# Performance work log

Hardware: AMD Instinct MI355X
Metric: run time of the kernel (lower is better)

The kernel has to match this reference:

```python
import jax, jax.numpy as jnp
import numpy as np

VOCAB, EMBED, CONV_C, HID, LABELS = 50257, 512, 512, 1024, 128
B, S = 32, 1024

def setup_inputs() -> dict:
    key = jax.random.key(0)
    ks = jax.random.split(key, 8)
    sc = lambda d: 1.0 / np.sqrt(d)
    return {
        "token_ids": jax.random.randint(ks[0], (B, S), 0, VOCAB),
        "emb_table": jax.random.normal(ks[1], (VOCAB, EMBED), jnp.float32) * 0.02,
        "conv_w": jax.random.normal(ks[2], (CONV_C, EMBED), jnp.float32) * sc(EMBED),
        "conv_b": jnp.zeros((CONV_C,), jnp.float32),
        "dec_w1": jax.random.normal(ks[3], (CONV_C, HID), jnp.float32) * sc(CONV_C),
        "dec_b1": jnp.zeros((HID,), jnp.float32),
        "dec_w2": jax.random.normal(ks[4], (HID, LABELS), jnp.float32) * sc(HID),
        "dec_b2": jnp.zeros((LABELS,), jnp.float32),
    }

def reference(token_ids, emb_table, conv_w, conv_b, dec_w1, dec_b1, dec_w2, dec_b2):
    # Embedding lookup: [B, S, E]
    x = emb_table[token_ids]
    # DocNN encoder on a length-1 sequence = kernel-1 conv + relu (+ trivial max-over-time)
    h = jax.nn.relu(jnp.einsum('bse,ce->bsc', x, conv_w) + conv_b)  # [B,S,C]
    # MLP decoder per word
    z = jax.nn.relu(jnp.einsum('bsc,ch->bsh', h, dec_w1) + dec_b1)  # [B,S,H]
    logits = jnp.einsum('bsh,hl->bsl', z, dec_w2) + dec_b2          # [B,S,L]
    # torch.cat over dim 0 of per-word outputs -> flat [B*S, L]
    return logits.reshape(-1, logits.shape[-1])
```

## Files before the change

### kernel.cpp

```cpp
#include <hip/hip_runtime.h>

typedef __bf16 bf16;
typedef __bf16 bf16x4 __attribute__((ext_vector_type(4)));
typedef __bf16 bf16x8 __attribute__((ext_vector_type(8)));
typedef float f32x4 __attribute__((ext_vector_type(4)));

#define NROWS 32768
#define EMBED 512
#define CONV_C 512
#define HID 1024
#define LABELS 128

__device__ inline void async16(const void* g, void* l) {
  __builtin_amdgcn_global_load_lds(
      (const __attribute__((address_space(1))) void*)g,
      (__attribute__((address_space(3))) void*)l, 16, 0, 0);
}

__device__ inline bf16x8 cvt8(const float* p) {
  f32x4 lo = *(const f32x4*)p;
  f32x4 hi = *(const f32x4*)(p + 4);
  bf16x8 r;
  r[0] = (bf16)lo[0]; r[1] = (bf16)lo[1]; r[2] = (bf16)lo[2]; r[3] = (bf16)lo[3];
  r[4] = (bf16)hi[0]; r[5] = (bf16)hi[1]; r[6] = (bf16)hi[2]; r[7] = (bf16)hi[3];
  return r;
}

__global__ void transpose_cvt(const float* __restrict__ in, bf16* __restrict__ out,
                              int K, int N) {
  __shared__ float t[64][65];
  int kb = blockIdx.x * 64, nb = blockIdx.y * 64;
  for (int i = threadIdx.x; i < 4096; i += 256) {
    int r = i >> 6, c = i & 63;
    t[r][c] = in[(size_t)(kb + r) * N + nb + c];
  }
  __syncthreads();
  for (int i = threadIdx.x; i < 4096; i += 256) {
    int r = i >> 6, c = i & 63;
    out[(size_t)(nb + r) * K + kb + c] = (bf16)t[c][r];
  }
}

__global__ __launch_bounds__(256) void gemm1_gather(
    const int* __restrict__ tok, const float* __restrict__ emb,
    const float* __restrict__ convw, const float* __restrict__ bias,
    bf16* __restrict__ out, int M, int N, int K) {
  __shared__ __attribute__((aligned(16))) float lAf[128 * 32];
  __shared__ __attribute__((aligned(16))) float lBf[128 * 32];
  const int tid = threadIdx.x;
  const int wave = tid >> 6, lane = tid & 63;
  const int m0 = blockIdx.x * 128, n0 = blockIdx.y * 128;
  const int wm = (wave & 1) * 64, wn = (wave >> 1) * 64;
  const int lrow = lane & 15, quad = lane >> 4;
  const int slot0 = wave * 64 + lane;
  const int cs4 = (slot0 & 7) * 4;
  const int rbase = slot0 >> 3;

  int trow[4];
#pragma unroll
  for (int c = 0; c < 4; ++c) trow[c] = tok[m0 + rbase + c * 32];

  const f32x4 zero4 = {0.f, 0.f, 0.f, 0.f};
  f32x4 acc[4][4];
#pragma unroll
  for (int i = 0; i < 4; ++i)
#pragma unroll
    for (int j = 0; j < 4; ++j) acc[i][j] = zero4;

  for (int k0 = 0; k0 < K; k0 += 32) {
#pragma unroll
    for (int c = 0; c < 4; ++c) {
      int row = rbase + c * 32;
      async16(emb + (size_t)trow[c] * EMBED + k0 + cs4,
              lAf + (size_t)(wave * 64 + c * 256) * 4);
      async16(convw + (size_t)(n0 + row) * K + k0 + cs4,
              lBf + (size_t)(wave * 64 + c * 256) * 4);
    }
    __syncthreads();

    bf16x8 a[4], b[4];
#pragma unroll
    for (int t = 0; t < 4; ++t) {
      a[t] = cvt8(lAf + (wm + t * 16 + lrow) * 32 + quad * 8);
      b[t] = cvt8(lBf + (wn + t * 16 + lrow) * 32 + quad * 8);
    }
#pragma unroll
    for (int mi = 0; mi < 4; ++mi)
#pragma unroll
      for (int ni = 0; ni < 4; ++ni)
        acc[mi][ni] =
            __builtin_amdgcn_mfma_f32_16x16x32_bf16(a[mi], b[ni], acc[mi][ni], 0, 0, 0);
    __syncthreads();
  }

#pragma unroll
  for (int mi = 0; mi < 4; ++mi) {
#pragma unroll
    for (int ni = 0; ni < 4; ++ni) {
      int col = n0 + wn + ni * 16 + lrow;
      float bv = bias[col];
#pragma unroll
      for (int r = 0; r < 4; ++r) {
        int row = m0 + wm + mi * 16 + quad * 4 + r;
        float v = acc[mi][ni][r] + bv;
        v = v > 0.f ? v : 0.f;
        out[(size_t)row * N + col] = (bf16)v;
      }
    }
  }
}

template <int BK, bool RELU, bool OUTBF>
__global__ __launch_bounds__(256) void gemm_bt(const bf16* __restrict__ A,
                                               const bf16* __restrict__ Bt,
                                               const float* __restrict__ bias,
                                               void* __restrict__ out,
                                               int M, int N, int K) {
  constexpr int GR = BK / 8;
  constexpr int ISS = 128 * GR / 256;
  __shared__ __attribute__((aligned(16))) bf16 lA[128 * BK];
  __shared__ __attribute__((aligned(16))) bf16 lB[128 * BK];
  const int tid = threadIdx.x;
  const int wave = tid >> 6, lane = tid & 63;
  const int m0 = blockIdx.x * 128, n0 = blockIdx.y * 128;
  const int wm = (wave & 1) * 64, wn = (wave >> 1) * 64;
  const int lrow = lane & 15, quad = lane >> 4;
  const int slot0 = wave * 64 + lane;

  const f32x4 zero4 = {0.f, 0.f, 0.f, 0.f};
  f32x4 acc[4][4];
#pragma unroll
  for (int i = 0; i < 4; ++i)
#pragma unroll
    for (int j = 0; j < 4; ++j) acc[i][j] = zero4;

  for (int k0 = 0; k0 < K; k0 += BK) {
#pragma unroll
    for (int c = 0; c < ISS; ++c) {
      int g = slot0 + c * 256;
      int row = g / GR, cs = g % GR;
      async16(A + (size_t)(m0 + row) * K + k0 + cs * 8,
              lA + (size_t)(wave * 64 + c * 256) * 8);
      async16(Bt + (size_t)(n0 + row) * K + k0 + cs * 8,
              lB + (size_t)(wave * 64 + c * 256) * 8);
    }
    __syncthreads();

#pragma unroll
    for (int ks = 0; ks < BK / 32; ++ks) {
      bf16x8 a[4], b[4];
#pragma unroll
      for (int t = 0; t < 4; ++t) {
        a[t] = *(const bf16x8*)(lA + (wm + t * 16 + lrow) * BK + ks * 32 + quad * 8);
        b[t] = *(const bf16x8*)(lB + (wn + t * 16 + lrow) * BK + ks * 32 + quad * 8);
      }
#pragma unroll
      for (int mi = 0; mi < 4; ++mi)
#pragma unroll
        for (int ni = 0; ni < 4; ++ni)
          acc[mi][ni] =
              __builtin_amdgcn_mfma_f32_16x16x32_bf16(a[mi], b[ni], acc[mi][ni], 0, 0, 0);
    }
    __syncthreads();
  }

#pragma unroll
  for (int mi = 0; mi < 4; ++mi) {
#pragma unroll
    for (int ni = 0; ni < 4; ++ni) {
      int col = n0 + wn + ni * 16 + lrow;
      float bv = bias[col];
#pragma unroll
      for (int r = 0; r < 4; ++r) {
        int row = m0 + wm + mi * 16 + quad * 4 + r;
        float v = acc[mi][ni][r] + bv;
        if (RELU) v = v > 0.f ? v : 0.f;
        if (OUTBF)
          ((bf16*)out)[(size_t)row * N + col] = (bf16)v;
        else
          ((float*)out)[(size_t)row * N + col] = v;
      }
    }
  }
}

__global__ __launch_bounds__(256) void gemm_bt64(const bf16* __restrict__ A,
                                                 const bf16* __restrict__ Bt,
                                                 const float* __restrict__ bias,
                                                 float* __restrict__ out,
                                                 int M, int N, int K) {
  __shared__ __attribute__((aligned(16))) bf16 lA[64 * 32];
  __shared__ __attribute__((aligned(16))) bf16 lB[128 * 32];
  const int tid = threadIdx.x;
  const int wave = tid >> 6, lane = tid & 63;
  const int m0 = blockIdx.x * 64, n0 = 0;
  const int wm = (wave & 1) * 32, wn = (wave >> 1) * 64;
  const int lrow = lane & 15, quad = lane >> 4;
  const int slot0 = wave * 64 + lane;

  const f32x4 zero4 = {0.f, 0.f, 0.f, 0.f};
  f32x4 acc[2][4];
#pragma unroll
  for (int i = 0; i < 2; ++i)
#pragma unroll
    for (int j = 0; j < 4; ++j) acc[i][j] = zero4;

  for (int k0 = 0; k0 < K; k0 += 32) {
    {
      int row = slot0 >> 2, cs = slot0 & 3;
      async16(A + (size_t)(m0 + row) * K + k0 + cs * 8,
              lA + (size_t)(wave * 64) * 8);
    }
#pragma unroll
    for (int c = 0; c < 2; ++c) {
      int g = slot0 + c * 256;
      int row = g >> 2, cs = g & 3;
      async16(Bt + (size_t)(n0 + row) * K + k0 + cs * 8,
              lB + (size_t)(wave * 64 + c * 256) * 8);
    }
    __syncthreads();

    bf16x8 a[2], b[4];
#pragma unroll
    for (int t = 0; t < 2; ++t)
      a[t] = *(const bf16x8*)(lA + (wm + t * 16 + lrow) * 32 + quad * 8);
#pragma unroll
    for (int t = 0; t < 4; ++t)
      b[t] = *(const bf16x8*)(lB + (wn + t * 16 + lrow) * 32 + quad * 8);
#pragma unroll
    for (int mi = 0; mi < 2; ++mi)
#pragma unroll
      for (int ni = 0; ni < 4; ++ni)
        acc[mi][ni] =
            __builtin_amdgcn_mfma_f32_16x16x32_bf16(a[mi], b[ni], acc[mi][ni], 0, 0, 0);
    __syncthreads();
  }

#pragma unroll
  for (int mi = 0; mi < 2; ++mi) {
#pragma unroll
    for (int ni = 0; ni < 4; ++ni) {
      int col = n0 + wn + ni * 16 + lrow;
      float bv = bias[col];
#pragma unroll
      for (int r = 0; r < 4; ++r) {
        int row = m0 + wm + mi * 16 + quad * 4 + r;
        out[(size_t)row * N + col] = acc[mi][ni][r] + bv;
      }
    }
  }
}


extern "C" void kernel_launch(void* const* d_in, const int* in_sizes, int n_in,
                              void* d_out, int out_size, void* d_ws, size_t ws_size,
                              hipStream_t stream) {
  const int* tok = (const int*)d_in[0];
  const float* emb = (const float*)d_in[1];
  const float* conv_w = (const float*)d_in[2];
  const float* conv_b = (const float*)d_in[3];
  const float* w1 = (const float*)d_in[4];
  const float* b1 = (const float*)d_in[5];
  const float* w2 = (const float*)d_in[6];
  const float* b2 = (const float*)d_in[7];
  float* out = (float*)d_out;

  char* ws = (char*)d_ws;
  bf16* wt1 = (bf16*)(ws);
  bf16* wt2 = (bf16*)(ws + (1u << 20));
  bf16* h = (bf16*)(ws + (2u << 20));
  bf16* z = (bf16*)(ws + (34u << 20));

  hipLaunchKernelGGL(transpose_cvt, dim3(8, 16), dim3(256), 0, stream,
                     w1, wt1, CONV_C, HID);
  hipLaunchKernelGGL(transpose_cvt, dim3(16, 2), dim3(256), 0, stream,
                     w2, wt2, HID, LABELS);

  hipLaunchKernelGGL(gemm1_gather, dim3(NROWS / 128, CONV_C / 128), dim3(256),
                     0, stream, tok, emb, conv_w, conv_b, h, NROWS, CONV_C, EMBED);
  hipLaunchKernelGGL((gemm_bt<64, true, true>), dim3(NROWS / 128, HID / 128), dim3(256),
                     0, stream, h, wt1, b1, (void*)z, NROWS, HID, CONV_C);
  hipLaunchKernelGGL(gemm_bt64, dim3(NROWS / 64, 1), dim3(256),
                     0, stream, z, wt2, b2, out, NROWS, LABELS, HID);
}
```

Baseline: 290.6 us.

## Pre-convert conv weights to bf16, XOR-swizzle gathered A tile, shrink GEMM2 K-tile

```diff
diff --git a/kernel.cpp b/kernel.cpp
--- a/kernel.cpp
+++ b/kernel.cpp
@@ -17,13 +17,23 @@
       (__attribute__((address_space(3))) void*)l, 16, 0, 0);
 }
 
-__device__ inline bf16x8 cvt8(const float* p) {
-  f32x4 lo = *(const f32x4*)p;
-  f32x4 hi = *(const f32x4*)(p + 4);
+__device__ inline bf16x8 cvt8_sw(const float* row, int o0, int o1) {
+  f32x4 lo = *(const f32x4*)(row + o0);
+  f32x4 hi = *(const f32x4*)(row + o1);
   bf16x8 r;
   r[0] = (bf16)lo[0]; r[1] = (bf16)lo[1]; r[2] = (bf16)lo[2]; r[3] = (bf16)lo[3];
   r[4] = (bf16)hi[0]; r[5] = (bf16)hi[1]; r[6] = (bf16)hi[2]; r[7] = (bf16)hi[3];
   return r;
+}
+
+
+__global__ void cvt_bf16(const float* __restrict__ in, bf16* __restrict__ out, int n) {
+  int i = (blockIdx.x * blockDim.x + threadIdx.x) * 4;
+  if (i >= n) return;
+  float4 v = *(const float4*)(in + i);
+  bf16x4 o;
+  o.x = (bf16)v.x; o.y = (bf16)v.y; o.z = (bf16)v.z; o.w = (bf16)v.w;
+  *(bf16x4*)(out + i) = o;
 }
 
 __global__ void transpose_cvt(const float* __restrict__ in, bf16* __restrict__ out,
@@ -43,22 +53,28 @@
 
 __global__ __launch_bounds__(256) void gemm1_gather(
     const int* __restrict__ tok, const float* __restrict__ emb,
-    const float* __restrict__ convw, const float* __restrict__ bias,
+    const bf16* __restrict__ convw, const float* __restrict__ bias,
     bf16* __restrict__ out, int M, int N, int K) {
   __shared__ __attribute__((aligned(16))) float lAf[128 * 32];
-  __shared__ __attribute__((aligned(16))) float lBf[128 * 32];
+  __shared__ __attribute__((aligned(16))) bf16 lB[128 * 32];
   const int tid = threadIdx.x;
   const int wave = tid >> 6, lane = tid & 63;
   const int m0 = blockIdx.x * 128, n0 = blockIdx.y * 128;
   const int wm = (wave & 1) * 64, wn = (wave >> 1) * 64;
   const int lrow = lane & 15, quad = lane >> 4;
   const int slot0 = wave * 64 + lane;
-  const int cs4 = (slot0 & 7) * 4;
-  const int rbase = slot0 >> 3;
-
+
+  int arow[4], acol[4];
+#pragma unroll
+  for (int c = 0; c < 4; ++c) {
+    int s = slot0 + c * 256;
+    int r = s >> 3, p = s & 7;
+    arow[c] = r;
+    acol[c] = (p ^ (r & 7)) * 4;
+  }
   int trow[4];
 #pragma unroll
-  for (int c = 0; c < 4; ++c) trow[c] = tok[m0 + rbase + c * 32];
+  for (int c = 0; c < 4; ++c) trow[c] = tok[m0 + arow[c]];
 
   const f32x4 zero4 = {0.f, 0.f, 0.f, 0.f};
   f32x4 acc[4][4];
@@ -69,20 +85,24 @@
 
   for (int k0 = 0; k0 < K; k0 += 32) {
 #pragma unroll
-    for (int c = 0; c < 4; ++c) {
-      int row = rbase + c * 32;
-      async16(emb + (size_t)trow[c] * EMBED + k0 + cs4,
+    for (int c = 0; c < 4; ++c)
+      async16(emb + (size_t)trow[c] * EMBED + k0 + acol[c],
               lAf + (size_t)(wave * 64 + c * 256) * 4);
-      async16(convw + (size_t)(n0 + row) * K + k0 + cs4,
-              lBf + (size_t)(wave * 64 + c * 256) * 4);
+#pragma unroll
+    for (int c = 0; c < 2; ++c) {
+      int s = slot0 + c * 256;
+      int r = s >> 2, cs = s & 3;
+      async16(convw + (size_t)(n0 + r) * K + k0 + cs * 8,
+              lB + (size_t)(wave * 64 + c * 256) * 8);
     }
     __syncthreads();
 
     bf16x8 a[4], b[4];
 #pragma unroll
     for (int t = 0; t < 4; ++t) {
-      a[t] = cvt8(lAf + (wm + t * 16 + lrow) * 32 + quad * 8);
-      b[t] = cvt8(lBf + (wn + t * 16 + lrow) * 32 + quad * 8);
+      int r = wm + t * 16 + lrow, sw = r & 7;
+      a[t] = cvt8_sw(lAf + r * 32, ((2 * quad) ^ sw) * 4, ((2 * quad + 1) ^ sw) * 4);
+      b[t] = *(const bf16x8*)(lB + (wn + t * 16 + lrow) * 32 + quad * 8);
     }
 #pragma unroll
     for (int mi = 0; mi < 4; ++mi)
@@ -110,16 +130,14 @@
   }
 }
 
-template <int BK, bool RELU, bool OUTBF>
+template <bool RELU, bool OUTBF>
 __global__ __launch_bounds__(256) void gemm_bt(const bf16* __restrict__ A,
                                                const bf16* __restrict__ Bt,
                                                const float* __restrict__ bias,
                                                void* __restrict__ out,
                                                int M, int N, int K) {
-  constexpr int GR = BK / 8;
-  constexpr int ISS = 128 * GR / 256;
-  __shared__ __attribute__((aligned(16))) bf16 lA[128 * BK];
-  __shared__ __attribute__((aligned(16))) bf16 lB[128 * BK];
+  __shared__ __attribute__((aligned(16))) bf16 lA[128 * 32];
+  __shared__ __attribute__((aligned(16))) bf16 lB[128 * 32];
   const int tid = threadIdx.x;
   const int wave = tid >> 6, lane = tid & 63;
   const int m0 = blockIdx.x * 128, n0 = blockIdx.y * 128;
@@ -134,11 +152,11 @@
 #pragma unroll
     for (int j = 0; j < 4; ++j) acc[i][j] = zero4;
 
-  for (int k0 = 0; k0 < K; k0 += BK) {
-#pragma unroll
-    for (int c = 0; c < ISS; ++c) {
+  for (int k0 = 0; k0 < K; k0 += 32) {
+#pragma unroll
+    for (int c = 0; c < 2; ++c) {
       int g = slot0 + c * 256;
-      int row = g / GR, cs = g % GR;
+      int row = g >> 2, cs = g & 3;
       async16(A + (size_t)(m0 + row) * K + k0 + cs * 8,
               lA + (size_t)(wave * 64 + c * 256) * 8);
       async16(Bt + (size_t)(n0 + row) * K + k0 + cs * 8,
@@ -146,21 +164,18 @@
     }
     __syncthreads();
 
-#pragma unroll
-    for (int ks = 0; ks < BK / 32; ++ks) {
-      bf16x8 a[4], b[4];
-#pragma unroll
-      for (int t = 0; t < 4; ++t) {
-        a[t] = *(const bf16x8*)(lA + (wm + t * 16 + lrow) * BK + ks * 32 + quad * 8);
-        b[t] = *(const bf16x8*)(lB + (wn + t * 16 + lrow) * BK + ks * 32 + quad * 8);
-      }
-#pragma unroll
-      for (int mi = 0; mi < 4; ++mi)
-#pragma unroll
-        for (int ni = 0; ni < 4; ++ni)
-          acc[mi][ni] =
-              __builtin_amdgcn_mfma_f32_16x16x32_bf16(a[mi], b[ni], acc[mi][ni], 0, 0, 0);
-    }
+    bf16x8 a[4], b[4];
+#pragma unroll
+    for (int t = 0; t < 4; ++t) {
+      a[t] = *(const bf16x8*)(lA + (wm + t * 16 + lrow) * 32 + quad * 8);
+      b[t] = *(const bf16x8*)(lB + (wn + t * 16 + lrow) * 32 + quad * 8);
+    }
+#pragma unroll
+    for (int mi = 0; mi < 4; ++mi)
+#pragma unroll
+      for (int ni = 0; ni < 4; ++ni)
+        acc[mi][ni] =
+            __builtin_amdgcn_mfma_f32_16x16x32_bf16(a[mi], b[ni], acc[mi][ni], 0, 0, 0);
     __syncthreads();
   }
 
@@ -266,19 +281,22 @@
   float* out = (float*)d_out;
 
   char* ws = (char*)d_ws;
-  bf16* wt1 = (bf16*)(ws);
-  bf16* wt2 = (bf16*)(ws + (1u << 20));
+  bf16* wtc = (bf16*)(ws);
+  bf16* wt1 = (bf16*)(ws + (1u << 19));
+  bf16* wt2 = (bf16*)(ws + 3 * (1u << 19));
   bf16* h = (bf16*)(ws + (2u << 20));
   bf16* z = (bf16*)(ws + (34u << 20));
 
+  hipLaunchKernelGGL(cvt_bf16, dim3(256), dim3(256), 0, stream,
+                     conv_w, wtc, CONV_C * EMBED);
   hipLaunchKernelGGL(transpose_cvt, dim3(8, 16), dim3(256), 0, stream,
                      w1, wt1, CONV_C, HID);
   hipLaunchKernelGGL(transpose_cvt, dim3(16, 2), dim3(256), 0, stream,
                      w2, wt2, HID, LABELS);
 
   hipLaunchKernelGGL(gemm1_gather, dim3(NROWS / 128, CONV_C / 128), dim3(256),
-                     0, stream, tok, emb, conv_w, conv_b, h, NROWS, CONV_C, EMBED);
-  hipLaunchKernelGGL((gemm_bt<64, true, true>), dim3(NROWS / 128, HID / 128), dim3(256),
+                     0, stream, tok, emb, wtc, conv_b, h, NROWS, CONV_C, EMBED);
+  hipLaunchKernelGGL((gemm_bt<true, true>), dim3(NROWS / 128, HID / 128), dim3(256),
                      0, stream, h, wt1, b1, (void*)z, NROWS, HID, CONV_C);
   hipLaunchKernelGGL(gemm_bt64, dim3(NROWS / 64, 1), dim3(256),
                      0, stream, z, wt2, b2, out, NROWS, LABELS, HID);
```

Result: faster. 270.3 us (-7.0%).
